# Optimization experiments

Measured on AMD Instinct MI355X. Metric: run time of the kernel, lower is better.

Reference implementation:

```python
import jax, jax.numpy as jnp
import numpy as np

B, N, E, T = 32768, 6, 6, 2  # batch graphs, nodes, edges (ring), edge types
H, DIN = 128, 3


def _ring_rel():
    # off_diag[i, (i+1)%N] = 1 -> edge e: sender i, receiver (i+1)%N
    send = np.arange(N)
    recv = (np.arange(N) + 1) % N
    eye = np.eye(N, dtype=np.float32)
    return jnp.asarray(eye[recv]), jnp.asarray(eye[send])  # rel_rec, rel_send [E,N]


def setup_inputs() -> dict:
    key = jax.random.key(0)
    ks = iter(jax.random.split(key, 40))
    rn = lambda shape, s=0.1: jax.random.normal(next(ks), shape, jnp.float32) * s
    rel_rec, rel_send = _ring_rel()
    inp = {
        'x': rn((B, N, DIN), 1.0),
        'rel_rec': rel_rec, 'rel_send': rel_send,
        'e1w1': rn((DIN, H)), 'e1b1': jnp.full((H,), 0.1), 'e1w2': rn((H, H)), 'e1b2': jnp.full((H,), 0.1),
        'e2w1': rn((2 * H, H)), 'e2b1': jnp.full((H,), 0.1), 'e2w2': rn((H, H)), 'e2b2': jnp.full((H,), 0.1),
        'e3w1': rn((H, H)), 'e3b1': jnp.full((H,), 0.1), 'e3w2': rn((H, H)), 'e3b2': jnp.full((H,), 0.1),
        'e4w1': rn((2 * H, H)), 'e4b1': jnp.full((H,), 0.1), 'e4w2': rn((H, H)), 'e4b2': jnp.full((H,), 0.1),
        'ew_out': rn((H, T)), 'eb_out': jnp.full((T,), 0.1),
        'd_msg_w1': rn((T, 2 * DIN, H)), 'd_msg_b1': rn((T, H), 0.01),
        'd_msg_w2': rn((T, H, H)), 'd_msg_b2': rn((T, H), 0.01),
        'd_out_w1': rn((DIN + H, H)), 'd_out_b1': rn((H,), 0.01),
        'd_out_w2': rn((H, H)), 'd_out_b2': rn((H,), 0.01),
        'd_out_w3': rn((H, DIN)), 'd_out_b3': rn((DIN,), 0.01),
    }
    return inp


def _mlp(h, w1, b1, w2, b2):
    # two-layer ELU MLP (dropout inactive at eval)
    return jax.nn.elu(jax.nn.elu(h @ w1 + b1) @ w2 + b2)


def reference(x, rel_rec, rel_send,
              e1w1, e1b1, e1w2, e1b2, e2w1, e2b1, e2w2, e2b2,
              e3w1, e3b1, e3w2, e3b2, e4w1, e4b1, e4w2, e4b2,
              ew_out, eb_out,
              d_msg_w1, d_msg_b1, d_msg_w2, d_msg_b2,
              d_out_w1, d_out_b1, d_out_w2, d_out_b2, d_out_w3, d_out_b3):
    node2edge = lambda h: jnp.concatenate(
        [jnp.einsum('en,bnh->beh', rel_rec, h), jnp.einsum('en,bnh->beh', rel_send, h)], axis=-1)

    # ---- GraphEncoder (factor=False) ----
    h = _mlp(x, e1w1, e1b1, e1w2, e1b2)                      # [B,N,H]
    he = _mlp(node2edge(h), e2w1, e2b1, e2w2, e2b2)          # [B,E,H]
    h2 = _mlp(he, e3w1, e3b1, e3w2, e3b2)                    # [B,E,H]
    h3 = _mlp(jnp.concatenate([h2, he], -1), e4w1, e4b1, e4w2, e4b2)
    logits = h3 @ ew_out + eb_out                            # [B,E,T]
    rel_type = jax.nn.softmax(logits, axis=-1)               # edge-type weights

    # ---- GraphDecoder single step (skip_first=False) ----
    recv = jnp.einsum('en,bnd->bed', rel_rec, x)             # [B,E,DIN]
    send = jnp.einsum('en,bnd->bed', rel_send, x)
    pre_msg = jnp.concatenate([recv, send], axis=-1)         # [B,E,2*DIN]
    # batched per-edge-type MLP: one grouped GEMM instead of a python loop of layers
    m = jax.nn.relu(jnp.einsum('bei,tih->bteh', pre_msg, d_msg_w1) + d_msg_b1[None, :, None, :])
    m = jax.nn.relu(jnp.einsum('bteh,tho->bteo', m, d_msg_w2) + d_msg_b2[None, :, None, :])
    all_msgs = jnp.einsum('bteh,bet->beh', m, rel_type)      # weight + accumulate over types
    agg_msgs = jnp.einsum('beh,en->bnh', all_msgs, rel_rec)  # edge -> node aggregation

    aug = jnp.concatenate([x, agg_msgs], axis=-1)            # [B,N,DIN+H]
    p = jax.nn.relu(aug @ d_out_w1 + d_out_b1)
    p = jax.nn.relu(p @ d_out_w2 + d_out_b2)
    p = p @ d_out_w3 + d_out_b3
    return x + p                                             # [B,N,DIN]
```

## Files before the change

kernel.cpp:

```cpp
#include <hip/hip_runtime.h>
#include <hip/hip_bf16.h>

typedef __bf16 bf16x8 __attribute__((ext_vector_type(8)));
typedef __bf16 bf16x4 __attribute__((ext_vector_type(4)));
typedef float floatx4 __attribute__((ext_vector_type(4)));

#define LDW 136
#define PXW 8

#define O_E1W2  0
#define O_E2W1  16384
#define O_E2W2  49152
#define O_E3W1  65536
#define O_E3W2  81920
#define O_E4W1  98304
#define O_E4W2  131072
#define O_DM2T0 147456
#define O_DM2T1 163840
#define O_DO1   180224
#define O_DO2   196608
#define O_EWOUT 212992
#define O_DW3   215040
#define O_E1W1P 217088
#define O_M1T0P 221184
#define O_M1T1P 225280
#define O_DO1XP 229376
#define WS_ELEMS 233472

__global__ void prep_kernel(const float* e1w2, const float* e2w1, const float* e2w2,
    const float* e3w1, const float* e3w2, const float* e4w1, const float* e4w2,
    const float* dmsg2, const float* dout1, const float* dout2,
    const float* ew_out, const float* dout_w3, const float* e1w1,
    const float* dmsg_w1, __hip_bfloat16* ws) {
  int idx = blockIdx.x * 256 + threadIdx.x;
  if (idx >= WS_ELEMS) return;
  float v;
  if (idx < O_E2W1)      { int l = idx;           v = e1w2[(l & 127) * 128 + (l >> 7)]; }
  else if (idx < O_E2W2) { int l = idx - O_E2W1;  v = e2w1[(l & 255) * 128 + (l >> 8)]; }
  else if (idx < O_E3W1) { int l = idx - O_E2W2;  v = e2w2[(l & 127) * 128 + (l >> 7)]; }
  else if (idx < O_E3W2) { int l = idx - O_E3W1;  v = e3w1[(l & 127) * 128 + (l >> 7)]; }
  else if (idx < O_E4W1) { int l = idx - O_E3W2;  v = e3w2[(l & 127) * 128 + (l >> 7)]; }
  else if (idx < O_E4W2) { int l = idx - O_E4W1;  v = e4w1[(l & 255) * 128 + (l >> 8)]; }
  else if (idx < O_DM2T0){ int l = idx - O_E4W2;  v = e4w2[(l & 127) * 128 + (l >> 7)]; }
  else if (idx < O_DM2T1){ int l = idx - O_DM2T0; v = dmsg2[(l & 127) * 128 + (l >> 7)]; }
  else if (idx < O_DO1)  { int l = idx - O_DM2T1; v = dmsg2[16384 + (l & 127) * 128 + (l >> 7)]; }
  else if (idx < O_DO2)  { int l = idx - O_DO1;   v = dout1[384 + (l & 127) * 128 + (l >> 7)]; }
  else if (idx < O_EWOUT){ int l = idx - O_DO2;   v = dout2[(l & 127) * 128 + (l >> 7)]; }
  else if (idx < O_DW3)  { int l = idx - O_EWOUT; int n = l >> 7;
                           v = (n < 2) ? ew_out[(l & 127) * 2 + n] : 0.f; }
  else if (idx < O_E1W1P){ int l = idx - O_DW3;   int n = l >> 7;
                           v = (n < 3) ? dout_w3[(l & 127) * 3 + n] : 0.f; }
  else if (idx < O_M1T0P){ int l = idx - O_E1W1P; int n = l >> 5, c = l & 31;
                           v = (c >= 3 && c < 6) ? e1w1[(c - 3) * 128 + n] : 0.f; }
  else if (idx < O_M1T1P){ int l = idx - O_M1T0P; int n = l >> 5, c = l & 31;
                           v = (c < 6) ? dmsg_w1[c * 128 + n] : 0.f; }
  else if (idx < O_DO1XP){ int l = idx - O_M1T1P; int n = l >> 5, c = l & 31;
                           v = (c < 6) ? dmsg_w1[768 + c * 128 + n] : 0.f; }
  else                   { int l = idx - O_DO1XP; int n = l >> 5, c = l & 31;
                           v = (c >= 3 && c < 6) ? dout1[(c - 3) * 128 + n] : 0.f; }
  ws[idx] = __float2bfloat16(v);
}

struct W4 { bf16x8 b[4]; };
struct W8 { bf16x8 b[8]; };
union PK { bf16x4 v; __hip_bfloat16 h[4]; };

__global__ __launch_bounds__(512, 4) void nri_fused(
    const float* __restrict__ x,
    const float* __restrict__ e1b1, const float* __restrict__ e1b2,
    const float* __restrict__ e2b1, const float* __restrict__ e2b2,
    const float* __restrict__ e3b1, const float* __restrict__ e3b2,
    const float* __restrict__ e4b1, const float* __restrict__ e4b2,
    const float* __restrict__ eb_out,
    const float* __restrict__ dmsg_b1, const float* __restrict__ dmsg_b2,
    const float* __restrict__ dout_b1, const float* __restrict__ dout_b2,
    const float* __restrict__ dout_b3,
    const __bf16* __restrict__ wt, float* __restrict__ out)
{
  const int tid  = threadIdx.x;
  const int wave = tid >> 6;
  const int lane = tid & 63;
  const int nl   = lane & 15;
  const int quad = lane >> 4;
  const int colb = wave * 16 + nl;
  const int cq   = wave * 16 + quad * 4;
  const int gx   = blockIdx.x * 288;

  __shared__ __align__(16) __hip_bfloat16 bufA[96 * LDW];
  __shared__ __align__(16) __hip_bfloat16 bufB[96 * LDW];
  __shared__ __align__(16) __hip_bfloat16 pxb[96 * PXW];
  __shared__ __hip_bfloat16 rtw[192];

  floatx4 b_s1 = *(const floatx4*)(e1b1 + cq);
  bf16x8 wk_s1 = *(const bf16x8*)(wt + O_E1W1P + colb * 32 + quad * 8);

  for (int i = tid; i < 96 * PXW; i += 512) {
    int row = i >> 3, c = i & 7;
    int e = row % 6;
    float v = 0.f;
    if (c < 3)      { int rr = row + ((e == 5) ? -5 : 1); v = x[gx + rr * 3 + c]; }
    else if (c < 6) v = x[gx + row * 3 + (c - 3)];
    pxb[i] = __float2bfloat16(v);
  }
  __syncthreads();

  auto initv = [&](floatx4 (&a)[6], floatx4 bv) {
#pragma unroll
    for (int mt = 0; mt < 6; ++mt) a[mt] = bv;
  };

  auto loadW128 = [&](int wofs) {
    W4 w;
    const __bf16* p = wt + wofs + colb * 128 + quad * 8;
#pragma unroll
    for (int ks = 0; ks < 4; ++ks) w.b[ks] = *(const bf16x8*)(p + ks * 32);
    return w;
  };
  auto loadW256 = [&](int wofs) {
    W8 w;
    const __bf16* p = wt + wofs + colb * 256 + quad * 8;
#pragma unroll
    for (int ks = 0; ks < 8; ++ks) w.b[ks] = *(const bf16x8*)(p + ks * 32);
    return w;
  };
  auto loadW256half = [&](int wofs, int kh) {
    W4 w;
    const __bf16* p = wt + wofs + colb * 256 + kh * 128 + quad * 8;
#pragma unroll
    for (int ks = 0; ks < 4; ++ks) w.b[ks] = *(const bf16x8*)(p + ks * 32);
    return w;
  };

  auto gemmP = [&](floatx4 (&acc)[6], const W4& w, const __hip_bfloat16* in) {
    const __bf16* ab = (const __bf16*)(const void*)in;
#pragma unroll
    for (int ks = 0; ks < 4; ++ks) {
      int kk = ks * 32 + quad * 8;
#pragma unroll
      for (int mt = 0; mt < 6; ++mt) {
        bf16x8 b = *(const bf16x8*)(ab + (mt * 16 + nl) * LDW + kk);
        acc[mt] = __builtin_amdgcn_mfma_f32_16x16x32_bf16(w.b[ks], b, acc[mt], 0, 0, 0);
      }
    }
  };
  auto gemmP2 = [&](floatx4 (&accA)[6], const W4& wA, floatx4 (&accB)[6],
                    const W4& wB, const __hip_bfloat16* in) {
    const __bf16* ab = (const __bf16*)(const void*)in;
#pragma unroll
    for (int ks = 0; ks < 4; ++ks) {
      int kk = ks * 32 + quad * 8;
#pragma unroll
      for (int mt = 0; mt < 6; ++mt) {
        bf16x8 b = *(const bf16x8*)(ab + (mt * 16 + nl) * LDW + kk);
        accA[mt] = __builtin_amdgcn_mfma_f32_16x16x32_bf16(wA.b[ks], b, accA[mt], 0, 0, 0);
        accB[mt] = __builtin_amdgcn_mfma_f32_16x16x32_bf16(wB.b[ks], b, accB[mt], 0, 0, 0);
      }
    }
  };
  auto gemm256P = [&](floatx4 (&acc)[6], const W8& w, const __hip_bfloat16* in) {
    int rofs0[6], rofs1[6];
#pragma unroll
    for (int mt = 0; mt < 6; ++mt) {
      int r = mt * 16 + nl;
      rofs1[mt] = r * LDW;
      int e = r % 6;
      rofs0[mt] = (r + ((e == 5) ? -5 : 1)) * LDW;
    }
    const __bf16* ab = (const __bf16*)(const void*)in;
#pragma unroll
    for (int ks = 0; ks < 8; ++ks) {
      int kk = (ks & 3) * 32 + quad * 8;
      const int* rofs = (ks < 4) ? rofs0 : rofs1;
#pragma unroll
      for (int mt = 0; mt < 6; ++mt) {
        bf16x8 b = *(const bf16x8*)(ab + rofs[mt] + kk);
        acc[mt] = __builtin_amdgcn_mfma_f32_16x16x32_bf16(w.b[ks], b, acc[mt], 0, 0, 0);
      }
    }
  };
  auto gemm32 = [&](floatx4 (&acc)[6], bf16x8 wfrag) {
    const __bf16* pb = (const __bf16*)(const void*)pxb;
#pragma unroll
    for (int mt = 0; mt < 6; ++mt) {
      bf16x8 b = {0, 0, 0, 0, 0, 0, 0, 0};
      if (quad == 0) b = *(const bf16x8*)(pb + (mt * 16 + nl) * PXW);
      acc[mt] = __builtin_amdgcn_mfma_f32_16x16x32_bf16(wfrag, b, acc[mt], 0, 0, 0);
    }
  };
  auto store_act = [&](floatx4 (&acc)[6], int act, __hip_bfloat16* ob) {
#pragma unroll
    for (int mt = 0; mt < 6; ++mt) {
      PK p;
#pragma unroll
      for (int r = 0; r < 4; ++r) {
        float z = acc[mt][r];
        if (act == 1) z = (z > 0.f) ? z : (__expf(z) - 1.f);
        else z = fmaxf(z, 0.f);
        p.h[r] = __float2bfloat16(z);
      }
      *(bf16x4*)((__bf16*)(void*)ob + (mt * 16 + nl) * LDW + cq) = p.v;
    }
  };

  floatx4 acc[6], acc2[6];

  initv(acc, b_s1); gemm32(acc, wk_s1);
  W4 w2 = loadW128(O_E1W2);
  floatx4 b_s2 = *(const floatx4*)(e1b2 + cq);
  store_act(acc, 1, bufA);
  __syncthreads();
  initv(acc, b_s2); gemmP(acc, w2, bufA);
  W8 w3 = loadW256(O_E2W1);
  floatx4 b_s3 = *(const floatx4*)(e2b1 + cq);
  store_act(acc, 1, bufB);
  __syncthreads();
  initv(acc, b_s3); gemm256P(acc, w3, bufB);
  W4 w4 = loadW128(O_E2W2);
  floatx4 b_s4 = *(const floatx4*)(e2b2 + cq);
  store_act(acc, 1, bufA);
  __syncthreads();
  initv(acc, b_s4); gemmP(acc, w4, bufA);
  W4 w5 = loadW128(O_E3W1);
  W4 w5b = loadW256half(O_E4W1, 1);
  floatx4 b_s5 = *(const floatx4*)(e3b1 + cq);
  floatx4 b2_s5 = *(const floatx4*)(e4b1 + cq);
  store_act(acc, 1, bufB);
  __syncthreads();
  initv(acc, b_s5); initv(acc2, b2_s5);
  gemmP2(acc, w5, acc2, w5b, bufB);
  W4 w6 = loadW128(O_E3W2);
  floatx4 b_s6 = *(const floatx4*)(e3b2 + cq);
  store_act(acc, 1, bufA);
  __syncthreads();
  initv(acc, b_s6); gemmP(acc, w6, bufA);
  W4 w7 = loadW256half(O_E4W1, 0);
  store_act(acc, 1, bufB);
  __syncthreads();
  gemmP(acc2, w7, bufB);
  W4 w8 = loadW128(O_E4W2);
  floatx4 b_s8 = *(const floatx4*)(e4b2 + cq);
  store_act(acc2, 1, bufA);
  __syncthreads();
  initv(acc, b_s8); gemmP(acc, w8, bufA);
  float ebv = (nl < 2) ? eb_out[nl] : 0.f;
  bf16x8 wk10a = *(const bf16x8*)(wt + O_M1T0P + colb * 32 + quad * 8);
  bf16x8 wk10b = *(const bf16x8*)(wt + O_M1T1P + colb * 32 + quad * 8);
  floatx4 b_m0 = *(const floatx4*)(dmsg_b1 + cq);
  floatx4 b_m1 = *(const floatx4*)(dmsg_b1 + 128 + cq);
  store_act(acc, 1, bufB);
  __syncthreads();

  if (wave < 6) {
    int tile = wave;
    floatx4 lg = {ebv, ebv, ebv, ebv};
    const __bf16* ab = (const __bf16*)(const void*)bufB;
    const __bf16* wp = wt + O_EWOUT + nl * 128 + quad * 8;
#pragma unroll
    for (int ks = 0; ks < 4; ++ks) {
      bf16x8 a = *(const bf16x8*)(ab + (tile * 16 + nl) * LDW + ks * 32 + quad * 8);
      bf16x8 b = *(const bf16x8*)(wp + ks * 32);
      lg = __builtin_amdgcn_mfma_f32_16x16x32_bf16(a, b, lg, 0, 0, 0);
    }
    if (nl < 2) {
#pragma unroll
      for (int r = 0; r < 4; ++r)
        rtw[(tile * 16 + quad * 4 + r) * 2 + nl] = __float2bfloat16(lg[r]);
    }
  }
  __syncthreads();

  if (tid < 96) {
    float l0 = __bfloat162float(rtw[tid * 2]);
    float l1 = __bfloat162float(rtw[tid * 2 + 1]);
    float mx = fmaxf(l0, l1);
    float ea = __expf(l0 - mx), eb = __expf(l1 - mx);
    float inv = 1.f / (ea + eb);
    rtw[tid * 2] = __float2bfloat16(ea * inv);
    rtw[tid * 2 + 1] = __float2bfloat16(eb * inv);
  }
  initv(acc, b_m0);  gemm32(acc, wk10a);  store_act(acc, 2, bufA);
  initv(acc2, b_m1); gemm32(acc2, wk10b); store_act(acc2, 2, bufB);
  W4 wm0 = loadW128(O_DM2T0);
  W4 wm1 = loadW128(O_DM2T1);
  floatx4 b_d0 = *(const floatx4*)(dmsg_b2 + cq);
  floatx4 b_d1 = *(const floatx4*)(dmsg_b2 + 128 + cq);
  __syncthreads();

  initv(acc, b_d0);  gemmP(acc, wm0, bufA);
  initv(acc2, b_d1); gemmP(acc2, wm1, bufB);
#pragma unroll
  for (int mt = 0; mt < 6; ++mt) {
    int row = mt * 16 + nl;
    float r0 = __bfloat162float(rtw[row * 2]);
    float r1 = __bfloat162float(rtw[row * 2 + 1]);
#pragma unroll
    for (int r = 0; r < 4; ++r)
      acc[mt][r] = r0 * fmaxf(acc[mt][r], 0.f) + r1 * fmaxf(acc2[mt][r], 0.f);
  }
  W4 wd1 = loadW128(O_DO1);
  bf16x8 wk13 = *(const bf16x8*)(wt + O_DO1XP + colb * 32 + quad * 8);
  floatx4 b_p1 = *(const floatx4*)(dout_b1 + cq);
  __syncthreads();

#pragma unroll
  for (int mt = 0; mt < 6; ++mt) {
    int row = mt * 16 + nl;
    int e = row % 6;
    int orow = row + ((e == 5) ? -5 : 1);
    PK p;
#pragma unroll
    for (int r = 0; r < 4; ++r) p.h[r] = __float2bfloat16(acc[mt][r]);
    *(bf16x4*)((__bf16*)(void*)bufA + orow * LDW + cq) = p.v;
  }
  __syncthreads();

  initv(acc, b_p1); gemmP(acc, wd1, bufA); gemm32(acc, wk13);
  W4 wd2 = loadW128(O_DO2);
  floatx4 b_p2 = *(const floatx4*)(dout_b2 + cq);
  store_act(acc, 2, bufB);
  __syncthreads();
  initv(acc, b_p2); gemmP(acc, wd2, bufB);
  float b3v = (nl < 3) ? dout_b3[nl] : 0.f;
  store_act(acc, 2, bufA);
  __syncthreads();

  if (wave < 6) {
    int tile = wave;
    floatx4 d = {b3v, b3v, b3v, b3v};
    const __bf16* ab = (const __bf16*)(const void*)bufA;
    const __bf16* wp = wt + O_DW3 + nl * 128 + quad * 8;
#pragma unroll
    for (int ks = 0; ks < 4; ++ks) {
      bf16x8 a = *(const bf16x8*)(ab + (tile * 16 + nl) * LDW + ks * 32 + quad * 8);
      bf16x8 b = *(const bf16x8*)(wp + ks * 32);
      d = __builtin_amdgcn_mfma_f32_16x16x32_bf16(a, b, d, 0, 0, 0);
    }
    if (nl < 3) {
#pragma unroll
      for (int r = 0; r < 4; ++r) {
        int row = tile * 16 + quad * 4 + r;
        out[gx + row * 3 + nl] = x[gx + row * 3 + nl] + d[r];
      }
    }
  }
}

extern "C" void kernel_launch(void* const* d_in, const int* in_sizes, int n_in,
                              void* d_out, int out_size, void* d_ws, size_t ws_size,
                              hipStream_t stream) {
  const float* x       = (const float*)d_in[0];
  const float* e1w1    = (const float*)d_in[3];
  const float* e1b1    = (const float*)d_in[4];
  const float* e1w2    = (const float*)d_in[5];
  const float* e1b2    = (const float*)d_in[6];
  const float* e2w1    = (const float*)d_in[7];
  const float* e2b1    = (const float*)d_in[8];
  const float* e2w2    = (const float*)d_in[9];
  const float* e2b2    = (const float*)d_in[10];
  const float* e3w1    = (const float*)d_in[11];
  const float* e3b1    = (const float*)d_in[12];
  const float* e3w2    = (const float*)d_in[13];
  const float* e3b2    = (const float*)d_in[14];
  const float* e4w1    = (const float*)d_in[15];
  const float* e4b1    = (const float*)d_in[16];
  const float* e4w2    = (const float*)d_in[17];
  const float* e4b2    = (const float*)d_in[18];
  const float* ew_out  = (const float*)d_in[19];
  const float* eb_out  = (const float*)d_in[20];
  const float* dmsg_w1 = (const float*)d_in[21];
  const float* dmsg_b1 = (const float*)d_in[22];
  const float* dmsg_w2 = (const float*)d_in[23];
  const float* dmsg_b2 = (const float*)d_in[24];
  const float* dout_w1 = (const float*)d_in[25];
  const float* dout_b1 = (const float*)d_in[26];
  const float* dout_w2 = (const float*)d_in[27];
  const float* dout_b2 = (const float*)d_in[28];
  const float* dout_w3 = (const float*)d_in[29];
  const float* dout_b3 = (const float*)d_in[30];

  prep_kernel<<<(WS_ELEMS + 255) / 256, 256, 0, stream>>>(
      e1w2, e2w1, e2w2, e3w1, e3w2, e4w1, e4w2, dmsg_w2, dout_w1, dout_w2,
      ew_out, dout_w3, e1w1, dmsg_w1, (__hip_bfloat16*)d_ws);

  nri_fused<<<32768 / 16, 512, 0, stream>>>(
      x, e1b1, e1b2, e2b1, e2b2, e3b1, e3b2, e4b1, e4b2, eb_out,
      dmsg_b1, dmsg_b2, dout_b1, dout_b2, dout_b3,
      (const __bf16*)d_ws, (float*)d_out);
}
```

Before: 255.1 us.

## Retile per-wave GEMM work into 48-row by 32-column blocks

Each wave previously owned a 16-column strip across all 96 rows, reading every activation row from LDS per k-step. Waves now own a 48-row by 32-column tile (2 row halves by 4 column groups), so each LDS activation fragment feeds two MFMAs and LDS read traffic per wave drops. One weight half is still held in registers and the other is streamed from global memory inside the k-loop, which keeps register pressure similar but adds global or L2 load latency inside the inner GEMM loop.

```diff
diff --git a/kernel.cpp b/kernel.cpp
--- a/kernel.cpp
+++ b/kernel.cpp
@@ -63,6 +63,7 @@
 
 struct W4 { bf16x8 b[4]; };
 struct W8 { bf16x8 b[8]; };
+struct B2 { floatx4 a, b; };
 union PK { bf16x4 v; __hip_bfloat16 h[4]; };
 
 __global__ __launch_bounds__(512, 4) void nri_fused(
@@ -82,17 +83,46 @@
   const int lane = tid & 63;
   const int nl   = lane & 15;
   const int quad = lane >> 4;
-  const int colb = wave * 16 + nl;
-  const int cq   = wave * 16 + quad * 4;
+  const int rb   = (wave >> 2) * 48;
+  const int cgb  = (wave & 3) * 32;
+  const int cq0  = cgb + quad * 4;
+  const int cq1  = cq0 + 16;
   const int gx   = blockIdx.x * 288;
+  const int rof0 = (rb + nl) * LDW;
+  const int rof1 = rof0 + 16 * LDW;
+  const int rof2 = rof0 + 32 * LDW;
 
   __shared__ __align__(16) __hip_bfloat16 bufA[96 * LDW];
   __shared__ __align__(16) __hip_bfloat16 bufB[96 * LDW];
   __shared__ __align__(16) __hip_bfloat16 pxb[96 * PXW];
   __shared__ __hip_bfloat16 rtw[192];
 
-  floatx4 b_s1 = *(const floatx4*)(e1b1 + cq);
-  bf16x8 wk_s1 = *(const bf16x8*)(wt + O_E1W1P + colb * 32 + quad * 8);
+  auto pW128 = [&](int wofs, int s) {
+    return wt + wofs + (cgb + s * 16 + nl) * 128 + quad * 8;
+  };
+  auto pW256 = [&](int wofs, int s, int kh) {
+    return wt + wofs + (cgb + s * 16 + nl) * 256 + kh * 128 + quad * 8;
+  };
+  auto ldw4 = [&](const __bf16* p) {
+    W4 w;
+#pragma unroll
+    for (int ks = 0; ks < 4; ++ks) w.b[ks] = *(const bf16x8*)(p + ks * 32);
+    return w;
+  };
+  auto ldw8 = [&](const __bf16* p) {
+    W8 w;
+#pragma unroll
+    for (int ks = 0; ks < 8; ++ks) w.b[ks] = *(const bf16x8*)(p + ks * 32);
+    return w;
+  };
+  auto loadB = [&](const float* p) {
+    B2 b; b.a = *(const floatx4*)(p + cq0); b.b = *(const floatx4*)(p + cq1);
+    return b;
+  };
+
+  B2 b_s1 = loadB(e1b1);
+  bf16x8 wk1a = *(const bf16x8*)(wt + O_E1W1P + (cgb + nl) * 32 + quad * 8);
+  bf16x8 wk1b = *(const bf16x8*)(wt + O_E1W1P + (cgb + 16 + nl) * 32 + quad * 8);
 
   for (int i = tid; i < 96 * PXW; i += 512) {
     int row = i >> 3, c = i & 7;
@@ -104,149 +134,130 @@
   }
   __syncthreads();
 
-  auto initv = [&](floatx4 (&a)[6], floatx4 bv) {
-#pragma unroll
-    for (int mt = 0; mt < 6; ++mt) a[mt] = bv;
-  };
-
-  auto loadW128 = [&](int wofs) {
-    W4 w;
-    const __bf16* p = wt + wofs + colb * 128 + quad * 8;
-#pragma unroll
-    for (int ks = 0; ks < 4; ++ks) w.b[ks] = *(const bf16x8*)(p + ks * 32);
-    return w;
-  };
-  auto loadW256 = [&](int wofs) {
-    W8 w;
-    const __bf16* p = wt + wofs + colb * 256 + quad * 8;
-#pragma unroll
-    for (int ks = 0; ks < 8; ++ks) w.b[ks] = *(const bf16x8*)(p + ks * 32);
-    return w;
-  };
-  auto loadW256half = [&](int wofs, int kh) {
-    W4 w;
-    const __bf16* p = wt + wofs + colb * 256 + kh * 128 + quad * 8;
-#pragma unroll
-    for (int ks = 0; ks < 4; ++ks) w.b[ks] = *(const bf16x8*)(p + ks * 32);
-    return w;
-  };
-
-  auto gemmP = [&](floatx4 (&acc)[6], const W4& w, const __hip_bfloat16* in) {
+  auto initv = [&](floatx4 (&a)[3][2], B2 bv) {
+#pragma unroll
+    for (int mt = 0; mt < 3; ++mt) { a[mt][0] = bv.a; a[mt][1] = bv.b; }
+  };
+
+  auto gemmP = [&](floatx4 (&acc)[3][2], const W4& w0, const __bf16* p1,
+                   const __hip_bfloat16* in) {
     const __bf16* ab = (const __bf16*)(const void*)in;
 #pragma unroll
     for (int ks = 0; ks < 4; ++ks) {
+      bf16x8 w1k = *(const bf16x8*)(p1 + ks * 32);
       int kk = ks * 32 + quad * 8;
-#pragma unroll
-      for (int mt = 0; mt < 6; ++mt) {
-        bf16x8 b = *(const bf16x8*)(ab + (mt * 16 + nl) * LDW + kk);
-        acc[mt] = __builtin_amdgcn_mfma_f32_16x16x32_bf16(w.b[ks], b, acc[mt], 0, 0, 0);
+      bf16x8 b0 = *(const bf16x8*)(ab + rof0 + kk);
+      bf16x8 b1 = *(const bf16x8*)(ab + rof1 + kk);
+      bf16x8 b2 = *(const bf16x8*)(ab + rof2 + kk);
+      acc[0][0] = __builtin_amdgcn_mfma_f32_16x16x32_bf16(w0.b[ks], b0, acc[0][0], 0, 0, 0);
+      acc[1][0] = __builtin_amdgcn_mfma_f32_16x16x32_bf16(w0.b[ks], b1, acc[1][0], 0, 0, 0);
+      acc[2][0] = __builtin_amdgcn_mfma_f32_16x16x32_bf16(w0.b[ks], b2, acc[2][0], 0, 0, 0);
+      acc[0][1] = __builtin_amdgcn_mfma_f32_16x16x32_bf16(w1k, b0, acc[0][1], 0, 0, 0);
+      acc[1][1] = __builtin_amdgcn_mfma_f32_16x16x32_bf16(w1k, b1, acc[1][1], 0, 0, 0);
+      acc[2][1] = __builtin_amdgcn_mfma_f32_16x16x32_bf16(w1k, b2, acc[2][1], 0, 0, 0);
+    }
+  };
+  auto gemm256P = [&](floatx4 (&acc)[3][2], const W8& w0, const __bf16* p1,
+                      const __hip_bfloat16* in) {
+    int rr[3];
+#pragma unroll
+    for (int mt = 0; mt < 3; ++mt) {
+      int r = rb + mt * 16 + nl;
+      int e = r % 6;
+      rr[mt] = (r + ((e == 5) ? -5 : 1)) * LDW;
+    }
+    const int rs[3] = {rof0, rof1, rof2};
+    const __bf16* ab = (const __bf16*)(const void*)in;
+#pragma unroll
+    for (int ks = 0; ks < 8; ++ks) {
+      bf16x8 w1k = *(const bf16x8*)(p1 + ks * 32);
+      int kk = (ks & 3) * 32 + quad * 8;
+      bf16x8 b0 = *(const bf16x8*)(ab + ((ks < 4) ? rr[0] : rs[0]) + kk);
+      bf16x8 b1 = *(const bf16x8*)(ab + ((ks < 4) ? rr[1] : rs[1]) + kk);
+      bf16x8 b2 = *(const bf16x8*)(ab + ((ks < 4) ? rr[2] : rs[2]) + kk);
+      acc[0][0] = __builtin_amdgcn_mfma_f32_16x16x32_bf16(w0.b[ks], b0, acc[0][0], 0, 0, 0);
+      acc[1][0] = __builtin_amdgcn_mfma_f32_16x16x32_bf16(w0.b[ks], b1, acc[1][0], 0, 0, 0);
+      acc[2][0] = __builtin_amdgcn_mfma_f32_16x16x32_bf16(w0.b[ks], b2, acc[2][0], 0, 0, 0);
+      acc[0][1] = __builtin_amdgcn_mfma_f32_16x16x32_bf16(w1k, b0, acc[0][1], 0, 0, 0);
+      acc[1][1] = __builtin_amdgcn_mfma_f32_16x16x32_bf16(w1k, b1, acc[1][1], 0, 0, 0);
+      acc[2][1] = __builtin_amdgcn_mfma_f32_16x16x32_bf16(w1k, b2, acc[2][1], 0, 0, 0);
+    }
+  };
+  auto gemm32 = [&](floatx4 (&acc)[3][2], bf16x8 f0, bf16x8 f1) {
+    const __bf16* pb = (const __bf16*)(const void*)pxb;
+#pragma unroll
+    for (int mt = 0; mt < 3; ++mt) {
+      bf16x8 b = {0, 0, 0, 0, 0, 0, 0, 0};
+      if (quad == 0) b = *(const bf16x8*)(pb + (rb + mt * 16 + nl) * PXW);
+      acc[mt][0] = __builtin_amdgcn_mfma_f32_16x16x32_bf16(f0, b, acc[mt][0], 0, 0, 0);
+      acc[mt][1] = __builtin_amdgcn_mfma_f32_16x16x32_bf16(f1, b, acc[mt][1], 0, 0, 0);
+    }
+  };
+  auto store_act = [&](floatx4 (&acc)[3][2], int act, __hip_bfloat16* ob) {
+    const int rs[3] = {rof0, rof1, rof2};
+#pragma unroll
+    for (int mt = 0; mt < 3; ++mt)
+#pragma unroll
+      for (int s = 0; s < 2; ++s) {
+        PK p;
+#pragma unroll
+        for (int r = 0; r < 4; ++r) {
+          float z = acc[mt][s][r];
+          if (act == 1) z = (z > 0.f) ? z : (__expf(z) - 1.f);
+          else z = fmaxf(z, 0.f);
+          p.h[r] = __float2bfloat16(z);
+        }
+        *(bf16x4*)((__bf16*)(void*)ob + rs[mt] + (s ? cq1 : cq0)) = p.v;
       }
-    }
-  };
-  auto gemmP2 = [&](floatx4 (&accA)[6], const W4& wA, floatx4 (&accB)[6],
-                    const W4& wB, const __hip_bfloat16* in) {
-    const __bf16* ab = (const __bf16*)(const void*)in;
-#pragma unroll
-    for (int ks = 0; ks < 4; ++ks) {
-      int kk = ks * 32 + quad * 8;
-#pragma unroll
-      for (int mt = 0; mt < 6; ++mt) {
-        bf16x8 b = *(const bf16x8*)(ab + (mt * 16 + nl) * LDW + kk);
-        accA[mt] = __builtin_amdgcn_mfma_f32_16x16x32_bf16(wA.b[ks], b, accA[mt], 0, 0, 0);
-        accB[mt] = __builtin_amdgcn_mfma_f32_16x16x32_bf16(wB.b[ks], b, accB[mt], 0, 0, 0);
-      }
-    }
-  };
-  auto gemm256P = [&](floatx4 (&acc)[6], const W8& w, const __hip_bfloat16* in) {
-    int rofs0[6], rofs1[6];
-#pragma unroll
-    for (int mt = 0; mt < 6; ++mt) {
-      int r = mt * 16 + nl;
-      rofs1[mt] = r * LDW;
-      int e = r % 6;
-      rofs0[mt] = (r + ((e == 5) ? -5 : 1)) * LDW;
-    }
-    const __bf16* ab = (const __bf16*)(const void*)in;
-#pragma unroll
-    for (int ks = 0; ks < 8; ++ks) {
-      int kk = (ks & 3) * 32 + quad * 8;
-      const int* rofs = (ks < 4) ? rofs0 : rofs1;
-#pragma unroll
-      for (int mt = 0; mt < 6; ++mt) {
-        bf16x8 b = *(const bf16x8*)(ab + rofs[mt] + kk);
-        acc[mt] = __builtin_amdgcn_mfma_f32_16x16x32_bf16(w.b[ks], b, acc[mt], 0, 0, 0);
-      }
-    }
-  };
-  auto gemm32 = [&](floatx4 (&acc)[6], bf16x8 wfrag) {
-    const __bf16* pb = (const __bf16*)(const void*)pxb;
-#pragma unroll
-    for (int mt = 0; mt < 6; ++mt) {
-      bf16x8 b = {0, 0, 0, 0, 0, 0, 0, 0};
-      if (quad == 0) b = *(const bf16x8*)(pb + (mt * 16 + nl) * PXW);
-      acc[mt] = __builtin_amdgcn_mfma_f32_16x16x32_bf16(wfrag, b, acc[mt], 0, 0, 0);
-    }
-  };
-  auto store_act = [&](floatx4 (&acc)[6], int act, __hip_bfloat16* ob) {
-#pragma unroll
-    for (int mt = 0; mt < 6; ++mt) {
-      PK p;
-#pragma unroll
-      for (int r = 0; r < 4; ++r) {
-        float z = acc[mt][r];
-        if (act == 1) z = (z > 0.f) ? z : (__expf(z) - 1.f);
-        else z = fmaxf(z, 0.f);
-        p.h[r] = __float2bfloat16(z);
-      }
-      *(bf16x4*)((__bf16*)(void*)ob + (mt * 16 + nl) * LDW + cq) = p.v;
-    }
-  };
-
-  floatx4 acc[6], acc2[6];
-
-  initv(acc, b_s1); gemm32(acc, wk_s1);
-  W4 w2 = loadW128(O_E1W2);
-  floatx4 b_s2 = *(const floatx4*)(e1b2 + cq);
+  };
+
+  floatx4 acc[3][2], acc2[3][2];
+
+  initv(acc, b_s1); gemm32(acc, wk1a, wk1b);
+  W4 w2 = ldw4(pW128(O_E1W2, 0));
+  B2 b_s2 = loadB(e1b2);
   store_act(acc, 1, bufA);
   __syncthreads();
-  initv(acc, b_s2); gemmP(acc, w2, bufA);
-  W8 w3 = loadW256(O_E2W1);
-  floatx4 b_s3 = *(const floatx4*)(e2b1 + cq);
+  initv(acc, b_s2); gemmP(acc, w2, pW128(O_E1W2, 1), bufA);
+  W8 w3 = ldw8(pW256(O_E2W1, 0, 0));
+  B2 b_s3 = loadB(e2b1);
   store_act(acc, 1, bufB);
   __syncthreads();
-  initv(acc, b_s3); gemm256P(acc, w3, bufB);
-  W4 w4 = loadW128(O_E2W2);
-  floatx4 b_s4 = *(const floatx4*)(e2b2 + cq);
+  initv(acc, b_s3); gemm256P(acc, w3, pW256(O_E2W1, 1, 0), bufB);
+  W4 w4 = ldw4(pW128(O_E2W2, 0));
+  B2 b_s4 = loadB(e2b2);
   store_act(acc, 1, bufA);
   __syncthreads();
-  initv(acc, b_s4); gemmP(acc, w4, bufA);
-  W4 w5 = loadW128(O_E3W1);
-  W4 w5b = loadW256half(O_E4W1, 1);
-  floatx4 b_s5 = *(const floatx4*)(e3b1 + cq);
-  floatx4 b2_s5 = *(const floatx4*)(e4b1 + cq);
+  initv(acc, b_s4); gemmP(acc, w4, pW128(O_E2W2, 1), bufA);
+  W4 w5 = ldw4(pW128(O_E3W1, 0));
+  W4 w5b = ldw4(pW256(O_E4W1, 0, 1));
+  B2 b_s5 = loadB(e3b1);
+  B2 b2_s5 = loadB(e4b1);
   store_act(acc, 1, bufB);
   __syncthreads();
-  initv(acc, b_s5); initv(acc2, b2_s5);
-  gemmP2(acc, w5, acc2, w5b, bufB);
-  W4 w6 = loadW128(O_E3W2);
-  floatx4 b_s6 = *(const floatx4*)(e3b2 + cq);
+  initv(acc, b_s5);  gemmP(acc, w5, pW128(O_E3W1, 1), bufB);
+  initv(acc2, b2_s5); gemmP(acc2, w5b, pW256(O_E4W1, 1, 1), bufB);
+  W4 w6 = ldw4(pW128(O_E3W2, 0));
+  B2 b_s6 = loadB(e3b2);
   store_act(acc, 1, bufA);
   __syncthreads();
-  initv(acc, b_s6); gemmP(acc, w6, bufA);
-  W4 w7 = loadW256half(O_E4W1, 0);
+  initv(acc, b_s6); gemmP(acc, w6, pW128(O_E3W2, 1), bufA);
+  W4 w7 = ldw4(pW256(O_E4W1, 0, 0));
   store_act(acc, 1, bufB);
   __syncthreads();
-  gemmP(acc2, w7, bufB);
-  W4 w8 = loadW128(O_E4W2);
-  floatx4 b_s8 = *(const floatx4*)(e4b2 + cq);
+  gemmP(acc2, w7, pW256(O_E4W1, 1, 0), bufB);
+  W4 w8 = ldw4(pW128(O_E4W2, 0));
+  B2 b_s8 = loadB(e4b2);
   store_act(acc2, 1, bufA);
   __syncthreads();
-  initv(acc, b_s8); gemmP(acc, w8, bufA);
+  initv(acc, b_s8); gemmP(acc, w8, pW128(O_E4W2, 1), bufA);
   float ebv = (nl < 2) ? eb_out[nl] : 0.f;
-  bf16x8 wk10a = *(const bf16x8*)(wt + O_M1T0P + colb * 32 + quad * 8);
-  bf16x8 wk10b = *(const bf16x8*)(wt + O_M1T1P + colb * 32 + quad * 8);
-  floatx4 b_m0 = *(const floatx4*)(dmsg_b1 + cq);
-  floatx4 b_m1 = *(const floatx4*)(dmsg_b1 + 128 + cq);
+  bf16x8 wk10a0 = *(const bf16x8*)(wt + O_M1T0P + (cgb + nl) * 32 + quad * 8);
+  bf16x8 wk10a1 = *(const bf16x8*)(wt + O_M1T0P + (cgb + 16 + nl) * 32 + quad * 8);
+  bf16x8 wk10b0 = *(const bf16x8*)(wt + O_M1T1P + (cgb + nl) * 32 + quad * 8);
+  bf16x8 wk10b1 = *(const bf16x8*)(wt + O_M1T1P + (cgb + 16 + nl) * 32 + quad * 8);
+  B2 b_m0 = loadB(dmsg_b1);
+  B2 b_m1 = loadB(dmsg_b1 + 128);
   store_act(acc, 1, bufB);
   __syncthreads();
 
@@ -278,48 +289,55 @@
     rtw[tid * 2] = __float2bfloat16(ea * inv);
     rtw[tid * 2 + 1] = __float2bfloat16(eb * inv);
   }
-  initv(acc, b_m0);  gemm32(acc, wk10a);  store_act(acc, 2, bufA);
-  initv(acc2, b_m1); gemm32(acc2, wk10b); store_act(acc2, 2, bufB);
-  W4 wm0 = loadW128(O_DM2T0);
-  W4 wm1 = loadW128(O_DM2T1);
-  floatx4 b_d0 = *(const floatx4*)(dmsg_b2 + cq);
-  floatx4 b_d1 = *(const floatx4*)(dmsg_b2 + 128 + cq);
-  __syncthreads();
-
-  initv(acc, b_d0);  gemmP(acc, wm0, bufA);
-  initv(acc2, b_d1); gemmP(acc2, wm1, bufB);
-#pragma unroll
-  for (int mt = 0; mt < 6; ++mt) {
-    int row = mt * 16 + nl;
+  initv(acc, b_m0);  gemm32(acc, wk10a0, wk10a1);  store_act(acc, 2, bufA);
+  initv(acc2, b_m1); gemm32(acc2, wk10b0, wk10b1); store_act(acc2, 2, bufB);
+  W4 wm0 = ldw4(pW128(O_DM2T0, 0));
+  W4 wm1 = ldw4(pW128(O_DM2T1, 0));
+  B2 b_d0 = loadB(dmsg_b2);
+  B2 b_d1 = loadB(dmsg_b2 + 128);
+  __syncthreads();
+
+  initv(acc, b_d0);  gemmP(acc, wm0, pW128(O_DM2T0, 1), bufA);
+  initv(acc2, b_d1); gemmP(acc2, wm1, pW128(O_DM2T1, 1), bufB);
+#pragma unroll
+  for (int mt = 0; mt < 3; ++mt) {
+    int row = rb + mt * 16 + nl;
     float r0 = __bfloat162float(rtw[row * 2]);
     float r1 = __bfloat162float(rtw[row * 2 + 1]);
 #pragma unroll
-    for (int r = 0; r < 4; ++r)
-      acc[mt][r] = r0 * fmaxf(acc[mt][r], 0.f) + r1 * fmaxf(acc2[mt][r], 0.f);
-  }
-  W4 wd1 = loadW128(O_DO1);
-  bf16x8 wk13 = *(const bf16x8*)(wt + O_DO1XP + colb * 32 + quad * 8);
-  floatx4 b_p1 = *(const floatx4*)(dout_b1 + cq);
-  __syncthreads();
-
-#pragma unroll
-  for (int mt = 0; mt < 6; ++mt) {
-    int row = mt * 16 + nl;
+    for (int s = 0; s < 2; ++s)
+#pragma unroll
+      for (int r = 0; r < 4; ++r)
+        acc[mt][s][r] = r0 * fmaxf(acc[mt][s][r], 0.f) + r1 * fmaxf(acc2[mt][s][r], 0.f);
+  }
+  W4 wd1 = ldw4(pW128(O_DO1, 0));
+  bf16x8 wk13a = *(const bf16x8*)(wt + O_DO1XP + (cgb + nl) * 32 + quad * 8);
+  bf16x8 wk13b = *(const bf16x8*)(wt + O_DO1XP + (cgb + 16 + nl) * 32 + quad * 8);
+  B2 b_p1 = loadB(dout_b1);
+  __syncthreads();
+
+#pragma unroll
+  for (int mt = 0; mt < 3; ++mt) {
+    int row = rb + mt * 16 + nl;
     int e = row % 6;
     int orow = row + ((e == 5) ? -5 : 1);
-    PK p;
-#pragma unroll
-    for (int r = 0; r < 4; ++r) p.h[r] = __float2bfloat16(acc[mt][r]);
-    *(bf16x4*)((__bf16*)(void*)bufA + orow * LDW + cq) = p.v;
-  }
-  __syncthreads();
-
-  initv(acc, b_p1); gemmP(acc, wd1, bufA); gemm32(acc, wk13);
-  W4 wd2 = loadW128(O_DO2);
-  floatx4 b_p2 = *(const floatx4*)(dout_b2 + cq);
+#pragma unroll
+    for (int s = 0; s < 2; ++s) {
+      PK p;
+#pragma unroll
+      for (int r = 0; r < 4; ++r) p.h[r] = __float2bfloat16(acc[mt][s][r]);
+      *(bf16x4*)((__bf16*)(void*)bufA + orow * LDW + (s ? cq1 : cq0)) = p.v;
+    }
+  }
+  __syncthreads();
+
+  initv(acc, b_p1); gemmP(acc, wd1, pW128(O_DO1, 1), bufA);
+  gemm32(acc, wk13a, wk13b);
+  W4 wd2 = ldw4(pW128(O_DO2, 0));
+  B2 b_p2 = loadB(dout_b2);
   store_act(acc, 2, bufB);
   __syncthreads();
-  initv(acc, b_p2); gemmP(acc, wd2, bufB);
+  initv(acc, b_p2); gemmP(acc, wd2, pW128(O_DO2, 1), bufB);
   float b3v = (nl < 3) ? dout_b3[nl] : 0.f;
   store_act(acc, 2, bufA);
   __syncthreads();
```

Measured after the change: 334.7 us. 1.31x slower.
